# Kernel optimization log

Hardware: AMD Instinct MI355X
Metric: run time of the kernel (lower is better)

## Reference

```python
import jax, jax.numpy as jnp
import numpy as np

NUM_HEADS = 16


def rotate_half(x):
    h = x.shape[-1] // 2
    return jnp.concatenate([-x[..., h:], x[..., :h]], axis=-1)


def setup_inputs() -> dict:
    key = jax.random.key(0)
    ks = jax.random.split(key, 8)
    S, dim, hd = 8192, 1280, 80
    n_seg = 8
    hidden_states = jax.random.normal(ks[0], (S, dim), dtype=jnp.float32)
    cu_seqlens = (jnp.arange(n_seg + 1, dtype=jnp.int32) * (S // n_seg))
    ang = jax.random.uniform(ks[1], (S, hd), dtype=jnp.float32) * (2.0 * np.pi)
    cos = jnp.cos(ang)
    sin = jnp.sin(ang)
    qkv_w = jax.random.normal(ks[2], (3 * dim, dim), dtype=jnp.float32) * (dim ** -0.5)
    qkv_b = jax.random.normal(ks[3], (3 * dim,), dtype=jnp.float32) * 0.02
    proj_w = jax.random.normal(ks[4], (dim, dim), dtype=jnp.float32) * (dim ** -0.5)
    proj_b = jax.random.normal(ks[5], (dim,), dtype=jnp.float32) * 0.02
    return {"hidden_states": hidden_states, "cu_seqlens": cu_seqlens,
            "cos": cos, "sin": sin, "qkv_w": qkv_w, "qkv_b": qkv_b,
            "proj_w": proj_w, "proj_b": proj_b}


def reference(hidden_states, cu_seqlens, cos, sin, qkv_w, qkv_b, proj_w, proj_b):
    S, dim = hidden_states.shape
    H = NUM_HEADS
    hd = dim // H
    scaling = hd ** -0.5

    # qkv projection: [S, 3*dim] -> [S, 3, H, hd]
    qkv = (hidden_states @ qkv_w.T + qkv_b).reshape(S, 3, H, hd)
    q, k, v = qkv[:, 0], qkv[:, 1], qkv[:, 2]  # each [S, H, hd]

    # RoPE in float32, cos/sin broadcast over heads
    c = cos[:, None, :].astype(jnp.float32)
    s = sin[:, None, :].astype(jnp.float32)
    qf, kf = q.astype(jnp.float32), k.astype(jnp.float32)
    q = (qf * c + rotate_half(qf) * s).astype(q.dtype)
    k = (kf * c + rotate_half(kf) * s).astype(k.dtype)

    # Block-diagonal varlen attention: equal-length segments -> batch dim
    lengths = np.diff(np.asarray(cu_seqlens))
    L = int(lengths[0])
    assert (lengths == L).all(), "reference assumes uniform segment lengths"
    B = lengths.shape[0]
    qb = q.reshape(B, L, H, hd)
    kb = k.reshape(B, L, H, hd)
    vb = v.reshape(B, L, H, hd)

    scores = jnp.einsum('blhd,bmhd->bhlm', qb, kb) * scaling
    probs = jax.nn.softmax(scores.astype(jnp.float32), axis=-1).astype(scores.dtype)
    out = jnp.einsum('bhlm,bmhd->blhd', probs, vb).reshape(S, dim)

    return out @ proj_w.T + proj_b
```

## Files before the change

kernel.cpp:

```cpp
#include <hip/hip_runtime.h>
#include <math.h>

typedef _Float16 f16;
typedef _Float16 half8 __attribute__((ext_vector_type(8)));
typedef _Float16 half4v __attribute__((ext_vector_type(4)));
typedef _Float16 half2v __attribute__((ext_vector_type(2)));
typedef float floatx4 __attribute__((ext_vector_type(4)));
typedef unsigned int u32;

#define AS1 __attribute__((address_space(1)))
#define AS3 __attribute__((address_space(3)))

__device__ __forceinline__ void stage16(f16* l, const f16* g) {
    __builtin_amdgcn_global_load_lds((const AS1 u32*)g, (AS3 u32*)l, 16, 0, 0);
}

__global__ __launch_bounds__(256) void cvt_f32_f16(const float* __restrict__ in,
                                                   f16* __restrict__ out, int n4) {
    int i = blockIdx.x * blockDim.x + threadIdx.x;
    if (i >= n4) return;
    float4 v = ((const float4*)in)[i];
    half4v h = {(f16)v.x, (f16)v.y, (f16)v.z, (f16)v.w};
    ((half4v*)out)[i] = h;
}

constexpr int GK = 1280;

__global__ __launch_bounds__(256) void gemm_nt(const f16* __restrict__ A,
                                               const f16* __restrict__ B,
                                               const float* __restrict__ bias,
                                               f16* __restrict__ outH,
                                               float* __restrict__ outF, int N) {
    __shared__ f16 As[128 * 32];
    __shared__ f16 Bs[128 * 32];
    const int t = threadIdx.x;
    const int lane = t & 63;
    const int w = t >> 6;
    const int wm = w & 1, wn = w >> 1;
    const int c16 = lane & 15, quad = lane >> 4;
    const size_t bm = blockIdx.x, bn = blockIdx.y;
    const f16* Ab = A + bm * 128 * GK;
    const f16* Bb = B + bn * 128 * GK;
    floatx4 acc[4][4] = {};
    const int c0 = t, c1 = t + 256;
    const int r0 = c0 >> 2, kc0 = ((c0 & 3) - (r0 >> 1)) & 3;
    const int r1 = c1 >> 2, kc1 = ((c1 & 3) - (r1 >> 1)) & 3;
    for (int k0 = 0; k0 < GK; k0 += 32) {
        stage16(As + c0 * 8, Ab + (size_t)r0 * GK + k0 + kc0 * 8);
        stage16(As + c1 * 8, Ab + (size_t)r1 * GK + k0 + kc1 * 8);
        stage16(Bs + c0 * 8, Bb + (size_t)r0 * GK + k0 + kc0 * 8);
        stage16(Bs + c1 * 8, Bb + (size_t)r1 * GK + k0 + kc1 * 8);
        __syncthreads();
        half8 af[4], bf[4];
#pragma unroll
        for (int i = 0; i < 4; i++) {
            const int row = wm * 64 + i * 16 + c16;
            af[i] = *(const half8*)(As + (4 * row + ((quad + (row >> 1)) & 3)) * 8);
        }
#pragma unroll
        for (int j = 0; j < 4; j++) {
            const int row = wn * 64 + j * 16 + c16;
            bf[j] = *(const half8*)(Bs + (4 * row + ((quad + (row >> 1)) & 3)) * 8);
        }
#pragma unroll
        for (int i = 0; i < 4; i++)
#pragma unroll
            for (int j = 0; j < 4; j++)
                acc[i][j] = __builtin_amdgcn_mfma_f32_16x16x32_f16(af[i], bf[j], acc[i][j], 0, 0, 0);
        __syncthreads();
    }
#pragma unroll
    for (int i = 0; i < 4; i++) {
#pragma unroll
        for (int j = 0; j < 4; j++) {
            const int col = (int)bn * 128 + wn * 64 + j * 16 + c16;
            const float bv = bias[col];
#pragma unroll
            for (int r = 0; r < 4; r++) {
                const size_t row = bm * 128 + wm * 64 + i * 16 + quad * 4 + r;
                const float v = acc[i][j][r] + bv;
                if (outH) outH[row * (size_t)N + col] = (f16)v;
                else      outF[row * (size_t)N + col] = v;
            }
        }
    }
}

#define QSCALE (0.11180339887498949f * 1.4426950408889634f)

__global__ __launch_bounds__(320) void rope_kernel(const f16* __restrict__ qkv,
                                                   const float* __restrict__ cosp,
                                                   const float* __restrict__ sinp,
                                                   f16* __restrict__ qb, f16* __restrict__ kb,
                                                   f16* __restrict__ vt) {
    constexpr int S = 8192;
    const int bs = blockIdx.x, h = blockIdx.y, t = threadIdx.x;
    const int sl = t / 5, g = t % 5;
    const int s = bs * 64 + sl;
    {
        const size_t base = (size_t)s * 3840 + h * 80 + g * 8;
        half8 qa = *(const half8*)(qkv + base);
        half8 qc = *(const half8*)(qkv + base + 40);
        half8 ka = *(const half8*)(qkv + base + 1280);
        half8 kc = *(const half8*)(qkv + base + 1320);
        const float* cp = cosp + (size_t)s * 80 + g * 8;
        const float* sp = sinp + (size_t)s * 80 + g * 8;
        half8 qo0, qo1, ko0, ko1;
#pragma unroll
        for (int j = 0; j < 8; j++) {
            float c0 = cp[j], c1 = cp[j + 40];
            float n0 = sp[j], n1 = sp[j + 40];
            float q0 = (float)qa[j], q1 = (float)qc[j];
            float k0 = (float)ka[j], k1 = (float)kc[j];
            qo0[j] = (f16)((q0 * c0 - q1 * n0) * QSCALE);
            qo1[j] = (f16)((q1 * c1 + q0 * n1) * QSCALE);
            ko0[j] = (f16)(k0 * c0 - k1 * n0);
            ko1[j] = (f16)(k1 * c1 + k0 * n1);
        }
        const size_t ob = ((size_t)h * S + s) * 96 + g * 8;
        *(half8*)(qb + ob)      = qo0;
        *(half8*)(qb + ob + 40) = qo1;
        *(half8*)(kb + ob)      = ko0;
        *(half8*)(kb + ob + 40) = ko1;
        if (g < 2) {
            half8 qp = {}, kp = {};
            if (g == 0) { qp[0] = (f16)(-8.0f); kp[0] = (f16)(1.0f); }
            const size_t pb = ((size_t)h * S + s) * 96 + 80 + g * 8;
            *(half8*)(qb + pb) = qp;
            *(half8*)(kb + pb) = kp;
        }
    }
    __shared__ f16 vls[64][81];
    for (int j = t; j < 64 * 80; j += 320) {
        int s2 = j / 80, d = j % 80;
        vls[s2][d] = qkv[((size_t)(bs * 64 + s2)) * 3840 + 2560 + h * 80 + d];
    }
    __syncthreads();
    for (int j = t; j < 64 * 80; j += 320) {
        int d = j >> 6, s2 = j & 63;
        vt[((size_t)(h * 80 + d)) * S + bs * 64 + s2] = vls[s2][d];
    }
}

__global__ __launch_bounds__(256, 3) void attn_kernel(const f16* __restrict__ qb,
                                                      const f16* __restrict__ kb,
                                                      const f16* __restrict__ vt,
                                                      const int* __restrict__ cu,
                                                      f16* __restrict__ out) {
    constexpr int S = 8192;
    __shared__ f16 Ks[2][64 * 96];
    __shared__ f16 Ps[128 * 72];
    const int t = threadIdx.x, lane = t & 63, w = t >> 6;
    const int c16 = lane & 15, quad = lane >> 4;
    const int qt = blockIdx.x, h = blockIdx.y, z = blockIdx.z;
    const int s0 = cu[z];

    half8 qf[2][3];
#pragma unroll
    for (int qt2 = 0; qt2 < 2; qt2++)
#pragma unroll
        for (int ks = 0; ks < 3; ks++)
            qf[qt2][ks] = *(const half8*)(qb + ((size_t)h * S + s0 + qt * 128 + w * 32 + qt2 * 16 + c16) * 96 + ks * 32 + quad * 8);

    const f16 ov = (c16 == 0) ? (f16)1.f : (f16)0.f;
    const half8 onesf = {ov, ov, ov, ov, ov, ov, ov, ov};

    const int sR = t >> 2;
    const int sK = ((t & 3) - (sR >> 1)) & 3;

    {
        const f16* Kg = kb + ((size_t)h * S + s0) * 96;
#pragma unroll
        for (int j = 0; j < 3; j++)
            stage16(&Ks[0][0] + (j * 256 + t) * 8, Kg + (size_t)sR * 96 + j * 32 + sK * 8);
    }
    __syncthreads();

    floatx4 o[6][2] = {};

    for (int kv = 0; kv < 16; kv++) {
        if (kv < 15) {
            const f16* Kg = kb + ((size_t)h * S + s0 + (kv + 1) * 64) * 96;
            f16* Kd = &Ks[(kv + 1) & 1][0];
#pragma unroll
            for (int j = 0; j < 3; j++)
                stage16(Kd + (j * 256 + t) * 8, Kg + (size_t)sR * 96 + j * 32 + sK * 8);
        }
        const f16* Kc = &Ks[kv & 1][0];
        floatx4 sc[4][2] = {};
#pragma unroll
        for (int ks = 0; ks < 3; ks++) {
            half8 kf[4];
#pragma unroll
            for (int mt = 0; mt < 4; mt++) {
                const int row = mt * 16 + c16;
                kf[mt] = *(const half8*)(Kc + (ks * 256 + 4 * row + ((quad + (row >> 1)) & 3)) * 8);
            }
#pragma unroll
            for (int qt2 = 0; qt2 < 2; qt2++)
#pragma unroll
                for (int mt = 0; mt < 4; mt++)
                    sc[mt][qt2] = __builtin_amdgcn_mfma_f32_16x16x32_f16(kf[mt], qf[qt2][ks], sc[mt][qt2], 0, 0, 0);
        }
#pragma unroll
        for (int qt2 = 0; qt2 < 2; qt2++) {
            const int q = w * 32 + qt2 * 16 + c16;
#pragma unroll
            for (int mt = 0; mt < 4; mt++) {
                half4v pv;
#pragma unroll
                for (int r = 0; r < 4; r++)
                    pv[r] = (f16)__builtin_amdgcn_exp2f(sc[mt][qt2][r]);
                *(half4v*)(Ps + q * 72 + mt * 16 + quad * 4) = pv;
            }
        }
#pragma unroll
        for (int ks = 0; ks < 2; ks++) {
            const f16* Vg = vt + (size_t)h * 80 * S + s0 + kv * 64 + ks * 32;
            half8 vf[5];
#pragma unroll
            for (int dt = 0; dt < 5; dt++)
                vf[dt] = *(const half8*)(Vg + (size_t)(dt * 16 + c16) * S + quad * 8);
#pragma unroll
            for (int qt2 = 0; qt2 < 2; qt2++) {
                const int q = w * 32 + qt2 * 16 + c16;
                half8 pf = *(const half8*)(Ps + q * 72 + ks * 32 + quad * 8);
#pragma unroll
                for (int dt = 0; dt < 5; dt++)
                    o[dt][qt2] = __builtin_amdgcn_mfma_f32_16x16x32_f16(vf[dt], pf, o[dt][qt2], 0, 0, 0);
                o[5][qt2] = __builtin_amdgcn_mfma_f32_16x16x32_f16(onesf, pf, o[5][qt2], 0, 0, 0);
            }
        }
        __syncthreads();
    }
#pragma unroll
    for (int qt2 = 0; qt2 < 2; qt2++) {
        const float l = __shfl(o[5][qt2][0], c16);
        const float inv = 1.f / l;
        const size_t srow = (size_t)s0 + qt * 128 + w * 32 + qt2 * 16 + c16;
#pragma unroll
        for (int dt = 0; dt < 5; dt++)
#pragma unroll
            for (int rp = 0; rp < 2; rp++) {
                half2v hv = {(f16)(o[dt][qt2][rp * 2] * inv), (f16)(o[dt][qt2][rp * 2 + 1] * inv)};
                *(half2v*)(out + srow * 1280 + h * 80 + dt * 16 + quad * 4 + rp * 2) = hv;
            }
    }
}

extern "C" void kernel_launch(void* const* d_in, const int* in_sizes, int n_in,
                              void* d_out, int out_size, void* d_ws, size_t ws_size,
                              hipStream_t stream) {
    const float* hidden = (const float*)d_in[0];
    const int* cu       = (const int*)d_in[1];
    const float* cosp   = (const float*)d_in[2];
    const float* sinp   = (const float*)d_in[3];
    const float* qkv_w  = (const float*)d_in[4];
    const float* qkv_b  = (const float*)d_in[5];
    const float* proj_w = (const float*)d_in[6];
    const float* proj_b = (const float*)d_in[7];
    float* out = (float*)d_out;

    constexpr size_t S = 8192, DIM = 1280, N3 = 3840;
    f16* A16   = (f16*)d_ws;
    f16* W16   = A16 + S * DIM;
    f16* P16   = W16 + N3 * DIM;
    f16* QKV16 = P16 + DIM * DIM;
    f16* QB    = QKV16 + S * N3;
    f16* KB    = QB + (size_t)16 * S * 96;
    f16* VT    = KB + (size_t)16 * S * 96;
    f16* AT16  = A16;

    {
        int n4 = (int)(S * DIM / 4);
        cvt_f32_f16<<<(n4 + 255) / 256, 256, 0, stream>>>(hidden, A16, n4);
    }
    {
        int n4 = (int)(N3 * DIM / 4);
        cvt_f32_f16<<<(n4 + 255) / 256, 256, 0, stream>>>(qkv_w, W16, n4);
    }
    {
        int n4 = (int)(DIM * DIM / 4);
        cvt_f32_f16<<<(n4 + 255) / 256, 256, 0, stream>>>(proj_w, P16, n4);
    }
    gemm_nt<<<dim3(64, 30), 256, 0, stream>>>(A16, W16, qkv_b, QKV16, nullptr, 3840);
    rope_kernel<<<dim3(128, 16), 320, 0, stream>>>(QKV16, cosp, sinp, QB, KB, VT);
    attn_kernel<<<dim3(8, 16, 8), 256, 0, stream>>>(QB, KB, VT, cu, AT16);
    gemm_nt<<<dim3(64, 10), 256, 0, stream>>>(AT16, P16, proj_b, nullptr, out, 1280);
}
```

Baseline: 397.5 us.

## Load B and K fragments directly from global into registers, double-buffer A

In the GEMM, the B operand is now read straight from global memory into registers and prefetched one k-step ahead, while the A tile is double-buffered in LDS. This halves shared memory use and overlaps loads with MFMA. In attention, the K tile is no longer staged through LDS; each wave reads K fragments from global (L2/cache) and the per-iteration barrier is removed. Occupancy hints are raised to 4 for both kernels. The risk is more redundant global traffic and register pressure, and un-hidden global latency for the K loads.

```diff
diff --git a/kernel.cpp b/kernel.cpp
--- a/kernel.cpp
+++ b/kernel.cpp
@@ -26,13 +26,12 @@
 
 constexpr int GK = 1280;
 
-__global__ __launch_bounds__(256) void gemm_nt(const f16* __restrict__ A,
-                                               const f16* __restrict__ B,
-                                               const float* __restrict__ bias,
-                                               f16* __restrict__ outH,
-                                               float* __restrict__ outF, int N) {
-    __shared__ f16 As[128 * 32];
-    __shared__ f16 Bs[128 * 32];
+__global__ __launch_bounds__(256, 4) void gemm_nt(const f16* __restrict__ A,
+                                                  const f16* __restrict__ B,
+                                                  const float* __restrict__ bias,
+                                                  f16* __restrict__ outH,
+                                                  float* __restrict__ outF, int N) {
+    __shared__ f16 As[2][128 * 32];
     const int t = threadIdx.x;
     const int lane = t & 63;
     const int w = t >> 6;
@@ -40,34 +39,44 @@
     const int c16 = lane & 15, quad = lane >> 4;
     const size_t bm = blockIdx.x, bn = blockIdx.y;
     const f16* Ab = A + bm * 128 * GK;
-    const f16* Bb = B + bn * 128 * GK;
+    const f16* Bw = B + (bn * 128 + wn * 64) * (size_t)GK;
     floatx4 acc[4][4] = {};
     const int c0 = t, c1 = t + 256;
     const int r0 = c0 >> 2, kc0 = ((c0 & 3) - (r0 >> 1)) & 3;
     const int r1 = c1 >> 2, kc1 = ((c1 & 3) - (r1 >> 1)) & 3;
+
+    stage16(&As[0][0] + c0 * 8, Ab + (size_t)r0 * GK + kc0 * 8);
+    stage16(&As[0][0] + c1 * 8, Ab + (size_t)r1 * GK + kc1 * 8);
+    half8 bcur[4], bnxt[4];
+#pragma unroll
+    for (int j = 0; j < 4; j++)
+        bcur[j] = *(const half8*)(Bw + (size_t)(j * 16 + c16) * GK + quad * 8);
+    __syncthreads();
+
+    int buf = 0;
     for (int k0 = 0; k0 < GK; k0 += 32) {
-        stage16(As + c0 * 8, Ab + (size_t)r0 * GK + k0 + kc0 * 8);
-        stage16(As + c1 * 8, Ab + (size_t)r1 * GK + k0 + kc1 * 8);
-        stage16(Bs + c0 * 8, Bb + (size_t)r0 * GK + k0 + kc0 * 8);
-        stage16(Bs + c1 * 8, Bb + (size_t)r1 * GK + k0 + kc1 * 8);
-        __syncthreads();
-        half8 af[4], bf[4];
+        if (k0 + 32 < GK) {
+            stage16(&As[buf ^ 1][0] + c0 * 8, Ab + (size_t)r0 * GK + k0 + 32 + kc0 * 8);
+            stage16(&As[buf ^ 1][0] + c1 * 8, Ab + (size_t)r1 * GK + k0 + 32 + kc1 * 8);
+#pragma unroll
+            for (int j = 0; j < 4; j++)
+                bnxt[j] = *(const half8*)(Bw + (size_t)(j * 16 + c16) * GK + k0 + 32 + quad * 8);
+        }
+        half8 af[4];
 #pragma unroll
         for (int i = 0; i < 4; i++) {
             const int row = wm * 64 + i * 16 + c16;
-            af[i] = *(const half8*)(As + (4 * row + ((quad + (row >> 1)) & 3)) * 8);
-        }
-#pragma unroll
-        for (int j = 0; j < 4; j++) {
-            const int row = wn * 64 + j * 16 + c16;
-            bf[j] = *(const half8*)(Bs + (4 * row + ((quad + (row >> 1)) & 3)) * 8);
+            af[i] = *(const half8*)(&As[buf][0] + (4 * row + ((quad + (row >> 1)) & 3)) * 8);
         }
 #pragma unroll
         for (int i = 0; i < 4; i++)
 #pragma unroll
             for (int j = 0; j < 4; j++)
-                acc[i][j] = __builtin_amdgcn_mfma_f32_16x16x32_f16(af[i], bf[j], acc[i][j], 0, 0, 0);
+                acc[i][j] = __builtin_amdgcn_mfma_f32_16x16x32_f16(af[i], bcur[j], acc[i][j], 0, 0, 0);
+#pragma unroll
+        for (int j = 0; j < 4; j++) bcur[j] = bnxt[j];
         __syncthreads();
+        buf ^= 1;
     }
 #pragma unroll
     for (int i = 0; i < 4; i++) {
@@ -142,13 +151,12 @@
     }
 }
 
-__global__ __launch_bounds__(256, 3) void attn_kernel(const f16* __restrict__ qb,
+__global__ __launch_bounds__(256, 4) void attn_kernel(const f16* __restrict__ qb,
                                                       const f16* __restrict__ kb,
                                                       const f16* __restrict__ vt,
                                                       const int* __restrict__ cu,
                                                       f16* __restrict__ out) {
     constexpr int S = 8192;
-    __shared__ f16 Ks[2][64 * 96];
     __shared__ f16 Ps[128 * 72];
     const int t = threadIdx.x, lane = t & 63, w = t >> 6;
     const int c16 = lane & 15, quad = lane >> 4;
@@ -165,37 +173,17 @@
     const f16 ov = (c16 == 0) ? (f16)1.f : (f16)0.f;
     const half8 onesf = {ov, ov, ov, ov, ov, ov, ov, ov};
 
-    const int sR = t >> 2;
-    const int sK = ((t & 3) - (sR >> 1)) & 3;
-
-    {
-        const f16* Kg = kb + ((size_t)h * S + s0) * 96;
-#pragma unroll
-        for (int j = 0; j < 3; j++)
-            stage16(&Ks[0][0] + (j * 256 + t) * 8, Kg + (size_t)sR * 96 + j * 32 + sK * 8);
-    }
-    __syncthreads();
-
     floatx4 o[6][2] = {};
 
     for (int kv = 0; kv < 16; kv++) {
-        if (kv < 15) {
-            const f16* Kg = kb + ((size_t)h * S + s0 + (kv + 1) * 64) * 96;
-            f16* Kd = &Ks[(kv + 1) & 1][0];
-#pragma unroll
-            for (int j = 0; j < 3; j++)
-                stage16(Kd + (j * 256 + t) * 8, Kg + (size_t)sR * 96 + j * 32 + sK * 8);
-        }
-        const f16* Kc = &Ks[kv & 1][0];
+        const f16* Kg = kb + ((size_t)h * S + s0 + kv * 64) * 96;
         floatx4 sc[4][2] = {};
 #pragma unroll
         for (int ks = 0; ks < 3; ks++) {
             half8 kf[4];
 #pragma unroll
-            for (int mt = 0; mt < 4; mt++) {
-                const int row = mt * 16 + c16;
-                kf[mt] = *(const half8*)(Kc + (ks * 256 + 4 * row + ((quad + (row >> 1)) & 3)) * 8);
-            }
+            for (int mt = 0; mt < 4; mt++)
+                kf[mt] = *(const half8*)(Kg + (size_t)(mt * 16 + c16) * 96 + ks * 32 + quad * 8);
 #pragma unroll
             for (int qt2 = 0; qt2 < 2; qt2++)
 #pragma unroll
@@ -231,7 +219,6 @@
                 o[5][qt2] = __builtin_amdgcn_mfma_f32_16x16x32_f16(onesf, pf, o[5][qt2], 0, 0, 0);
             }
         }
-        __syncthreads();
     }
 #pragma unroll
     for (int qt2 = 0; qt2 < 2; qt2++) {
```

Result: slower. 568.6 us (+43.0%).

## Pre-pack weights into MFMA fragment order and load B directly from global

Applied to the files above, without the earlier changes.

Weight conversion now writes fp16 weights in a per-wave fragment-packed layout, so the GEMM loads B operands straight from global memory into registers as contiguous 16-byte reads per lane. The B shared-memory tile and its staging are removed. This halves LDS traffic and LDS usage per block, which may raise occupancy. In exchange, B reuse across the two wm waves is lost, so global/L2 B traffic doubles, and the direct loads are issued before the barrier with no prefetch to hide their latency.

```diff
diff --git a/kernel.cpp b/kernel.cpp
--- a/kernel.cpp
+++ b/kernel.cpp
@@ -24,15 +24,32 @@
     ((half4v*)out)[i] = h;
 }
 
+__global__ __launch_bounds__(256) void pack_w(const float* __restrict__ Wf,
+                                              f16* __restrict__ Wp) {
+    const int p = blockIdx.x * 256 + threadIdx.x;
+    const int lane = p & 63;
+    const int j = (p >> 6) & 3;
+    const int sk = p >> 8;
+    const int k0 = sk % 40;
+    const int slab = sk / 40;
+    const int row = slab * 64 + j * 16 + (lane & 15);
+    const int col = k0 * 32 + (lane >> 4) * 8;
+    const float* src = Wf + (size_t)row * 1280 + col;
+    float4 a = *(const float4*)src;
+    float4 b = *(const float4*)(src + 4);
+    half8 h = {(f16)a.x, (f16)a.y, (f16)a.z, (f16)a.w,
+               (f16)b.x, (f16)b.y, (f16)b.z, (f16)b.w};
+    *(half8*)(Wp + (size_t)p * 8) = h;
+}
+
 constexpr int GK = 1280;
 
 __global__ __launch_bounds__(256) void gemm_nt(const f16* __restrict__ A,
-                                               const f16* __restrict__ B,
+                                               const f16* __restrict__ Bp,
                                                const float* __restrict__ bias,
                                                f16* __restrict__ outH,
                                                float* __restrict__ outF, int N) {
     __shared__ f16 As[128 * 32];
-    __shared__ f16 Bs[128 * 32];
     const int t = threadIdx.x;
     const int lane = t & 63;
     const int w = t >> 6;
@@ -40,27 +57,25 @@
     const int c16 = lane & 15, quad = lane >> 4;
     const size_t bm = blockIdx.x, bn = blockIdx.y;
     const f16* Ab = A + bm * 128 * GK;
-    const f16* Bb = B + bn * 128 * GK;
+    const f16* Bw = Bp + (size_t)(bn * 2 + wn) * (40 * 4 * 64 * 8);
     floatx4 acc[4][4] = {};
     const int c0 = t, c1 = t + 256;
     const int r0 = c0 >> 2, kc0 = ((c0 & 3) - (r0 >> 1)) & 3;
     const int r1 = c1 >> 2, kc1 = ((c1 & 3) - (r1 >> 1)) & 3;
-    for (int k0 = 0; k0 < GK; k0 += 32) {
+    for (int k0i = 0; k0i < 40; k0i++) {
+        const int k0 = k0i * 32;
         stage16(As + c0 * 8, Ab + (size_t)r0 * GK + k0 + kc0 * 8);
         stage16(As + c1 * 8, Ab + (size_t)r1 * GK + k0 + kc1 * 8);
-        stage16(Bs + c0 * 8, Bb + (size_t)r0 * GK + k0 + kc0 * 8);
-        stage16(Bs + c1 * 8, Bb + (size_t)r1 * GK + k0 + kc1 * 8);
+        half8 bf[4];
+#pragma unroll
+        for (int j = 0; j < 4; j++)
+            bf[j] = *(const half8*)(Bw + (((size_t)k0i * 4 + j) * 64 + lane) * 8);
         __syncthreads();
-        half8 af[4], bf[4];
+        half8 af[4];
 #pragma unroll
         for (int i = 0; i < 4; i++) {
             const int row = wm * 64 + i * 16 + c16;
             af[i] = *(const half8*)(As + (4 * row + ((quad + (row >> 1)) & 3)) * 8);
-        }
-#pragma unroll
-        for (int j = 0; j < 4; j++) {
-            const int row = wn * 64 + j * 16 + c16;
-            bf[j] = *(const half8*)(Bs + (4 * row + ((quad + (row >> 1)) & 3)) * 8);
         }
 #pragma unroll
         for (int i = 0; i < 4; i++)
@@ -263,9 +278,9 @@
 
     constexpr size_t S = 8192, DIM = 1280, N3 = 3840;
     f16* A16   = (f16*)d_ws;
-    f16* W16   = A16 + S * DIM;
-    f16* P16   = W16 + N3 * DIM;
-    f16* QKV16 = P16 + DIM * DIM;
+    f16* WP16  = A16 + S * DIM;
+    f16* PP16  = WP16 + N3 * DIM;
+    f16* QKV16 = PP16 + DIM * DIM;
     f16* QB    = QKV16 + S * N3;
     f16* KB    = QB + (size_t)16 * S * 96;
     f16* VT    = KB + (size_t)16 * S * 96;
@@ -275,16 +290,10 @@
         int n4 = (int)(S * DIM / 4);
         cvt_f32_f16<<<(n4 + 255) / 256, 256, 0, stream>>>(hidden, A16, n4);
     }
-    {
-        int n4 = (int)(N3 * DIM / 4);
-        cvt_f32_f16<<<(n4 + 255) / 256, 256, 0, stream>>>(qkv_w, W16, n4);
-    }
-    {
-        int n4 = (int)(DIM * DIM / 4);
-        cvt_f32_f16<<<(n4 + 255) / 256, 256, 0, stream>>>(proj_w, P16, n4);
-    }
-    gemm_nt<<<dim3(64, 30), 256, 0, stream>>>(A16, W16, qkv_b, QKV16, nullptr, 3840);
+    pack_w<<<(int)(N3 * DIM / 8 / 256), 256, 0, stream>>>(qkv_w, WP16);
+    pack_w<<<(int)(DIM * DIM / 8 / 256), 256, 0, stream>>>(proj_w, PP16);
+    gemm_nt<<<dim3(64, 30), 256, 0, stream>>>(A16, WP16, qkv_b, QKV16, nullptr, 3840);
     rope_kernel<<<dim3(128, 16), 320, 0, stream>>>(QKV16, cosp, sinp, QB, KB, VT);
     attn_kernel<<<dim3(8, 16, 8), 256, 0, stream>>>(QB, KB, VT, cu, AT16);
-    gemm_nt<<<dim3(64, 10), 256, 0, stream>>>(AT16, P16, proj_b, nullptr, out, 1280);
-}
+    gemm_nt<<<dim3(64, 10), 256, 0, stream>>>(AT16, PP16, proj_b, nullptr, out, 1280);
+}
```

Result: no change. 399.4 us (+0.5%).
